# Kernel tuning notes

Measured on AMD Instinct MI355X. Metric: run time of the kernel, lower is better.

Reference implementation:

```python
import math
import jax, jax.numpy as jnp
import numpy as np

B, T, D, H = 2, 2048, 768, 12
DH = D // H
EPS = 1e-5


def setup_inputs() -> dict:
    key = jax.random.key(0)
    ks = jax.random.split(key, 8)
    s = 0.02
    x = jax.random.normal(ks[0], (B, T, D), dtype=jnp.float32)
    lengths = jax.random.randint(ks[1], (B,), T // 2, T + 1)
    lengths = lengths.at[0].set(T)  # ensure max(lengths)==T (static shape)
    return {
        'x': x,
        'lengths': lengths,
        'w_qkv': jax.random.normal(ks[2], (D, 3 * D), dtype=jnp.float32) * s,
        'b_qkv': jnp.zeros((3 * D,), jnp.float32),
        'w_proj': jax.random.normal(ks[3], (D, D), dtype=jnp.float32) * s,
        'b_proj': jnp.zeros((D,), jnp.float32),
        'ln1_g': jnp.ones((D,), jnp.float32),
        'ln1_b': jnp.zeros((D,), jnp.float32),
        'w_fc': jax.random.normal(ks[4], (D, 4 * D), dtype=jnp.float32) * s,
        'b_fc': jnp.zeros((4 * D,), jnp.float32),
        'w_out': jax.random.normal(ks[5], (4 * D, D), dtype=jnp.float32) * s,
        'b_out': jnp.zeros((D,), jnp.float32),
        'ln2_g': jnp.ones((D,), jnp.float32),
        'ln2_b': jnp.zeros((D,), jnp.float32),
    }


def _gelu(x):
    c = math.sqrt(2.0 / math.pi)
    return 0.5 * x * (1.0 + jnp.tanh(c * (x + 0.044715 * x * x * x)))


def _layernorm(x, g, b):
    mu = jnp.mean(x, axis=-1, keepdims=True)
    var = jnp.mean(jnp.square(x - mu), axis=-1, keepdims=True)
    return (x - mu) * jax.lax.rsqrt(var + EPS) * g + b


def _block(x, lengths, w_qkv, b_qkv, w_proj, b_proj, ln1_g, ln1_b,
           w_fc, b_fc, w_out, b_out, ln2_g, ln2_b):
    dt = x.dtype
    # [B, T] validity mask from ragged lengths
    pos = jnp.arange(T)
    mask = (pos[None, :] < lengths[:, None]).astype(dt)

    # --- SeqMultiHeadAttention (scale=False) ---
    qkv = x @ w_qkv + b_qkv  # [B, T, 3D]
    q, k, v = jnp.split(qkv, 3, axis=-1)

    def split_heads(t):  # [B,T,D] -> [B,H,T,DH]
        return t.reshape(B, T, H, DH).transpose(0, 2, 1, 3)

    q, k, v = split_heads(q), split_heads(k), split_heads(v)
    w = jnp.einsum('bhqd,bhkd->bhqk', q, k)  # [B,H,T,T]
    amask = (mask[:, None, :, None] * mask[:, None, None, :])  # [B,1,T,T]
    w = w * amask + (-1e9) * (1.0 - amask)
    w = jax.nn.softmax(w, axis=-1) * amask
    a = jnp.einsum('bhqk,bhkd->bhqd', w, v)  # [B,H,T,DH]
    a = a.transpose(0, 2, 1, 3).reshape(B, T, D)
    a = a @ w_proj + b_proj

    # --- SeqLayerNorm 1: pack/unpack == per-position LN, padding zeroed ---
    n = _layernorm(x + a, ln1_g, ln1_b) * mask[..., None]

    # --- MLP (gelu) ---
    m = _gelu(n @ w_fc + b_fc) @ w_out + b_out

    # --- SeqLayerNorm 2 ---
    h = _layernorm(n + m, ln2_g, ln2_b) * mask[..., None]
    return h


def reference(x, lengths, w_qkv, b_qkv, w_proj, b_proj, ln1_g, ln1_b,
              w_fc, b_fc, w_out, b_out, ln2_g, ln2_b):
    return _block(x, lengths, w_qkv, b_qkv, w_proj, b_proj, ln1_g, ln1_b,
                  w_fc, b_fc, w_out, b_out, ln2_g, ln2_b)
```

## Files before the change

kernel.cpp:

```cpp
#include <hip/hip_runtime.h>
#include <hip/hip_bf16.h>
#include <math.h>

constexpr int Bc  = 2;
constexpr int Tc  = 2048;
constexpr int Dc  = 768;
constexpr int Hc  = 12;
constexpr int DHc = 64;
constexpr int M_ROWS = Bc * Tc;
constexpr int D3  = 3 * Dc;
constexpr int D4  = 4 * Dc;

typedef __attribute__((ext_vector_type(8))) short short8;
typedef __attribute__((ext_vector_type(4))) float f32x4;

__device__ __forceinline__ unsigned short f2bf(float v) {
    union { __hip_bfloat16 b; unsigned short u; } cv;
    cv.b = __float2bfloat16(v);
    return cv.u;
}
__device__ __forceinline__ float bf2f(unsigned short u) {
    union { __hip_bfloat16 b; unsigned short u; } cv;
    cv.u = u;
    return __bfloat162float(cv.b);
}
__device__ __forceinline__ void bsplit(float v, unsigned short& h, unsigned short& l) {
    h = f2bf(v);
    l = f2bf(v - bf2f(h));
}

__device__ __forceinline__ float gelu_f(float x) {
    const float c = 0.79788456080286535588f;
    return 0.5f * x * (1.0f + tanhf(c * (x + 0.044715f * x * x * x)));
}

__device__ __forceinline__ void glds16(const unsigned short* g, unsigned short* l) {
    __builtin_amdgcn_global_load_lds(
        (const __attribute__((address_space(1))) void*)g,
        (__attribute__((address_space(3))) void*)l, 16, 0, 0);
}

__device__ __forceinline__ void tcast8(
    const float* __restrict__ w, int ldw,
    unsigned short* __restrict__ th, int K, int N, int idx)
{
    const int n  = idx % N;
    const int k0 = (idx / N) * 8;
    unsigned short hv[8];
#pragma unroll
    for (int j = 0; j < 8; ++j)
        hv[j] = f2bf(w[(size_t)(k0 + j) * ldw + n]);
    const size_t o = (size_t)n * K + k0;
    *(ushort4*)(th + o)     = make_ushort4(hv[0], hv[1], hv[2], hv[3]);
    *(ushort4*)(th + o + 4) = make_ushort4(hv[4], hv[5], hv[6], hv[7]);
}

__global__ __launch_bounds__(256) void prepare_kernel(
    const float* __restrict__ x,
    const float* __restrict__ w_qkv, const float* __restrict__ w_proj,
    const float* __restrict__ w_fc,  const float* __restrict__ w_out,
    unsigned short* __restrict__ xh,
    unsigned short* __restrict__ wqkvT, unsigned short* __restrict__ wprojT,
    unsigned short* __restrict__ wfcT,  unsigned short* __restrict__ woutT)
{
    int id = blockIdx.x * 256 + threadIdx.x;
    if (id < 786432) {
        const float4 v = *(const float4*)(x + (size_t)id * 4);
        *(ushort4*)(xh + (size_t)id * 4) =
            make_ushort4(f2bf(v.x), f2bf(v.y), f2bf(v.z), f2bf(v.w));
        return;
    }
    id -= 786432;
    if (id < 221184) { tcast8(w_qkv, D3, wqkvT, Dc, D3, id); return; }
    id -= 221184;
    if (id < 73728)  { tcast8(w_proj, Dc, wprojT, Dc, Dc, id); return; }
    id -= 73728;
    if (id < 294912) { tcast8(w_fc, D4, wfcT, Dc, D4, id); return; }
    id -= 294912;
    tcast8(w_out, Dc, woutT, D4, Dc, id);
}

template <int TM, int MODE>
__global__ __launch_bounds__(256) void gemm_bf16(
    const unsigned short* __restrict__ A,
    const unsigned short* __restrict__ B,
    const float* __restrict__ bias,
    float* __restrict__ C, unsigned short* __restrict__ Cb,
    int M, int N, int K)
{
    constexpr int MT  = TM / 32;
    constexpr int ISS = TM / 32 + 4;
    __shared__ unsigned short Ash[2][TM * 64];
    __shared__ unsigned short Bsh[2][128 * 64];

    const int tid  = threadIdx.x;
    const int n0   = blockIdx.x * 128;
    const int m0   = blockIdx.y * TM;
    const int wave = tid >> 6;
    const int lane = tid & 63;
    const int wm   = (wave >> 1) * (TM / 2);
    const int wn   = (wave & 1) * 64;
    const int lrow = lane & 15;
    const int quad = lane >> 4;
    const int swz  = lrow & 7;

    f32x4 acc[MT][4];
    const f32x4 zero = {0.f, 0.f, 0.f, 0.f};
#pragma unroll
    for (int i = 0; i < MT; ++i)
#pragma unroll
        for (int j = 0; j < 4; ++j) acc[i][j] = zero;

    const int l8r  = lane >> 3;
    const int csel = ((lane & 7) ^ l8r) * 8;

    const int nsteps = K >> 6;

    auto stage = [&](int t, int b) {
        const int ks = t << 6;
#pragma unroll
        for (int j = 0; j < TM / 32; ++j) {
            const int rbase = wave * (TM / 4) + j * 8;
            glds16(A + (size_t)(m0 + rbase + l8r) * K + ks + csel,
                   &Ash[b][rbase * 64]);
        }
#pragma unroll
        for (int j = 0; j < 4; ++j) {
            const int rbase = wave * 32 + j * 8;
            glds16(B + (size_t)(n0 + rbase + l8r) * K + ks + csel,
                   &Bsh[b][rbase * 64]);
        }
    };

    stage(0, 0);
    stage(1, 1);

    for (int s = 0; s < nsteps; ++s) {
        const int cur = s & 1;

        if (s + 1 < nsteps) {
            asm volatile("s_waitcnt vmcnt(%0)" :: "i"(ISS) : "memory");
        } else {
            asm volatile("s_waitcnt vmcnt(0)" ::: "memory");
        }
        __builtin_amdgcn_s_barrier();

#pragma unroll
        for (int kk = 0; kk < 2; ++kk) {
            short8 fa[MT], fb[4];
            const int cl = kk * 4 + quad;
            const int pc = (cl ^ swz) * 8;
#pragma unroll
            for (int t = 0; t < MT; ++t)
                fa[t] = *(const short8*)&Ash[cur][(wm + t * 16 + lrow) * 64 + pc];
#pragma unroll
            for (int t = 0; t < 4; ++t)
                fb[t] = *(const short8*)&Bsh[cur][(wn + t * 16 + lrow) * 64 + pc];
#pragma unroll
            for (int mt = 0; mt < MT; ++mt)
#pragma unroll
                for (int nt = 0; nt < 4; ++nt)
                    acc[mt][nt] = __builtin_amdgcn_mfma_f32_16x16x32_bf16(
                        fa[mt], fb[nt], acc[mt][nt], 0, 0, 0);
        }

        __builtin_amdgcn_s_barrier();
        if (s + 2 < nsteps) stage(s + 2, cur);
    }

#pragma unroll
    for (int mt = 0; mt < MT; ++mt) {
        const int rowb = m0 + wm + mt * 16 + quad * 4;
#pragma unroll
        for (int nt = 0; nt < 4; ++nt) {
            const int col = n0 + wn + nt * 16 + lrow;
            const float bv = bias[col];
#pragma unroll
            for (int r = 0; r < 4; ++r) {
                const size_t ci = (size_t)(rowb + r) * N + col;
                if (MODE == 0) {
                    C[ci] = acc[mt][nt][r] + bv;
                } else if (MODE == 1) {
                    Cb[ci] = f2bf(gelu_f(acc[mt][nt][r] + bv));
                } else {
                    Cb[ci] = f2bf(acc[mt][nt][r] + bv);
                }
            }
        }
    }
}

constexpr int KS  = 72;
constexpr int PS2 = 72;

__global__ __launch_bounds__(256) void flash_attn_bf16(
    const unsigned short* __restrict__ qkv,
    const int* __restrict__ lengths,
    unsigned short* __restrict__ oh)
{
    __shared__ unsigned short Kh[64 * KS];
    __shared__ unsigned short Vt[64 * KS];
    __shared__ unsigned short PfU[64 * PS2];

    const int tid  = threadIdx.x;
    const int wave = tid >> 6;
    const int lane = tid & 63;
    const int m    = lane & 15;
    const int quad = lane >> 4;

    const int nqt = Tc / 64;
    const int qt  = blockIdx.x % nqt;
    const int bh  = blockIdx.x / nqt;
    const int hh  = bh % Hc;
    const int b   = bh / Hc;
    const int len = lengths[b];
    const int q0  = qt * 64;
    const size_t rs = (size_t)D3;
    const unsigned short* base = qkv + (size_t)b * Tc * rs;
    const int qcol = hh * DHc;
    const int kcol = Dc + hh * DHc;
    const int vcol = 2 * Dc + hh * DHc;

    if (q0 >= len) {
#pragma unroll
        for (int r = 0; r < 4; ++r) {
            const int qrow = q0 + wave * 16 + quad * 4 + r;
            const size_t ob = (size_t)(b * Tc + qrow) * Dc + hh * DHc + m;
#pragma unroll
            for (int nt = 0; nt < 4; ++nt) oh[ob + nt * 16] = 0;
        }
        return;
    }

    const int ktEnd = (min(len, Tc) + 63) >> 6;

    short8 Qf[2];
#pragma unroll
    for (int ch = 0; ch < 2; ++ch) {
        const size_t ga = (size_t)(q0 + wave * 16 + m) * rs + qcol + ch * 32 + quad * 8;
        const short8 q8 = *(const short8*)&base[ga];
        short8 qs;
#pragma unroll
        for (int j = 0; j < 8; ++j)
            qs[j] = (short)f2bf(bf2f((unsigned short)q8[j]) * 1.44269504088896f);
        Qf[ch] = qs;
    }

    f32x4 Oacc[4];
    const f32x4 zero = {0.f, 0.f, 0.f, 0.f};
#pragma unroll
    for (int nt = 0; nt < 4; ++nt) Oacc[nt] = zero;
    float lrow[4] = {0.f, 0.f, 0.f, 0.f};

    const int kr0 = tid >> 3,          kc0 = (tid & 7) * 8;
    const int kr1 = (tid + 256) >> 3,  kc1 = ((tid + 256) & 7) * 8;
    const int pk  = (tid >> 4) * 4;
    const int pd  = (tid & 15) * 4;
    const int vswz = ((pk >> 3) ^ ((pd >> 2) & 7)) * 8 + (pk & 7);

    short8  pK0, pK1;
    ushort4 pV0, pV1, pV2, pV3;
    {
        pK0 = *(const short8*)&base[(size_t)kr0 * rs + kcol + kc0];
        pK1 = *(const short8*)&base[(size_t)kr1 * rs + kcol + kc1];
        pV0 = *(const ushort4*)&base[(size_t)(pk + 0) * rs + vcol + pd];
        pV1 = *(const ushort4*)&base[(size_t)(pk + 1) * rs + vcol + pd];
        pV2 = *(const ushort4*)&base[(size_t)(pk + 2) * rs + vcol + pd];
        pV3 = *(const ushort4*)&base[(size_t)(pk + 3) * rs + vcol + pd];
    }

    for (int kt = 0; kt < ktEnd; ++kt) {
        const int kbase = kt * 64;
        __syncthreads();

        *(short8*)&Kh[kr0 * KS + kc0] = pK0;
        *(short8*)&Kh[kr1 * KS + kc1] = pK1;
        *(ushort4*)&Vt[(pd + 0) * KS + vswz] = make_ushort4(pV0.x, pV1.x, pV2.x, pV3.x);
        *(ushort4*)&Vt[(pd + 1) * KS + vswz] = make_ushort4(pV0.y, pV1.y, pV2.y, pV3.y);
        *(ushort4*)&Vt[(pd + 2) * KS + vswz] = make_ushort4(pV0.z, pV1.z, pV2.z, pV3.z);
        *(ushort4*)&Vt[(pd + 3) * KS + vswz] = make_ushort4(pV0.w, pV1.w, pV2.w, pV3.w);
        __syncthreads();

        if (kt + 1 < ktEnd) {
            const int nb = kbase + 64;
            pK0 = *(const short8*)&base[(size_t)(nb + kr0) * rs + kcol + kc0];
            pK1 = *(const short8*)&base[(size_t)(nb + kr1) * rs + kcol + kc1];
            pV0 = *(const ushort4*)&base[(size_t)(nb + pk + 0) * rs + vcol + pd];
            pV1 = *(const ushort4*)&base[(size_t)(nb + pk + 1) * rs + vcol + pd];
            pV2 = *(const ushort4*)&base[(size_t)(nb + pk + 2) * rs + vcol + pd];
            pV3 = *(const ushort4*)&base[(size_t)(nb + pk + 3) * rs + vcol + pd];
        }

        f32x4 S4[4];
#pragma unroll
        for (int nt = 0; nt < 4; ++nt) S4[nt] = zero;
#pragma unroll
        for (int ch = 0; ch < 2; ++ch)
#pragma unroll
            for (int nt = 0; nt < 4; ++nt) {
                const short8 k8 = *(const short8*)&Kh[(nt * 16 + m) * KS + ch * 32 + quad * 8];
                S4[nt] = __builtin_amdgcn_mfma_f32_16x16x32_bf16(Qf[ch], k8, S4[nt], 0, 0, 0);
            }

        if (kbase + 64 > len) {
#pragma unroll
            for (int nt = 0; nt < 4; ++nt)
                if (kbase + nt * 16 + m >= len) {
#pragma unroll
                    for (int r = 0; r < 4; ++r) S4[nt][r] = -1e30f;
                }
        }

#pragma unroll
        for (int nt = 0; nt < 4; ++nt)
#pragma unroll
            for (int r = 0; r < 4; ++r) {
                const float p = __builtin_amdgcn_exp2f(S4[nt][r]);
                lrow[r] += p;
                PfU[(wave * 16 + quad * 4 + r) * PS2 + nt * 16 + m] = f2bf(p);
            }

#pragma unroll
        for (int ch = 0; ch < 2; ++ch) {
            const short8 P8 = *(const short8*)&PfU[(wave * 16 + m) * PS2 + ch * 32 + quad * 8];
#pragma unroll
            for (int nt = 0; nt < 4; ++nt) {
                const int pchunk = ((ch * 4 + quad) ^ ((nt * 4 + (m >> 2)) & 7)) * 8;
                const short8 v8 = *(const short8*)&Vt[(nt * 16 + m) * KS + pchunk];
                Oacc[nt] = __builtin_amdgcn_mfma_f32_16x16x32_bf16(P8, v8, Oacc[nt], 0, 0, 0);
            }
        }
    }

#pragma unroll
    for (int r = 0; r < 4; ++r) {
#pragma unroll
        for (int sh = 8; sh >= 1; sh >>= 1)
            lrow[r] += __shfl_xor(lrow[r], sh);
    }

#pragma unroll
    for (int r = 0; r < 4; ++r) {
        const int qrow = q0 + wave * 16 + quad * 4 + r;
        const size_t ob = (size_t)(b * Tc + qrow) * Dc + hh * DHc + m;
        if (qrow < len) {
            const float inv = 1.0f / lrow[r];
#pragma unroll
            for (int nt = 0; nt < 4; ++nt)
                oh[ob + nt * 16] = f2bf(Oacc[nt][r] * inv);
        } else {
#pragma unroll
            for (int nt = 0; nt < 4; ++nt)
                oh[ob + nt * 16] = 0;
        }
    }
}

__global__ __launch_bounds__(256) void ln_split_kernel(
    const float* __restrict__ X, const float* __restrict__ Y,
    const float* __restrict__ g, const float* __restrict__ beta,
    const int* __restrict__ lengths,
    unsigned short* __restrict__ outh, unsigned short* __restrict__ outl)
{
    __shared__ float red[4];
    const int row = blockIdx.x;
    const int b = row / Tc, t = row % Tc;
    const int len = lengths[b];
    const size_t basei = (size_t)row * Dc;
    const int tid = threadIdx.x;

    if (t >= len) {
        for (int j = tid; j < Dc; j += 256) { outh[basei + j] = 0; outl[basei + j] = 0; }
        return;
    }

    float v[3];
    float s = 0.f;
#pragma unroll
    for (int j = 0; j < 3; ++j) {
        int idx = tid + j * 256;
        v[j] = X[basei + idx] + Y[basei + idx];
        s += v[j];
    }
    const int lane = tid % 64, wid = tid / 64;
#pragma unroll
    for (int sh = 32; sh >= 1; sh >>= 1) s += __shfl_xor(s, sh);
    if (lane == 0) red[wid] = s;
    __syncthreads();
    s = red[0] + red[1] + red[2] + red[3];
    const float mu = s * (1.0f / Dc);

    float vs = 0.f;
#pragma unroll
    for (int j = 0; j < 3; ++j) { float dv = v[j] - mu; vs += dv * dv; }
    __syncthreads();
#pragma unroll
    for (int sh = 32; sh >= 1; sh >>= 1) vs += __shfl_xor(vs, sh);
    if (lane == 0) red[wid] = vs;
    __syncthreads();
    vs = red[0] + red[1] + red[2] + red[3];
    const float rstd = rsqrtf(vs * (1.0f / Dc) + 1e-5f);

#pragma unroll
    for (int j = 0; j < 3; ++j) {
        int idx = tid + j * 256;
        const float ov = (v[j] - mu) * rstd * g[idx] + beta[idx];
        unsigned short hh, ll;
        bsplit(ov, hh, ll);
        outh[basei + idx] = hh;
        outl[basei + idx] = ll;
    }
}

__global__ __launch_bounds__(256) void ln2_kernel(
    const unsigned short* __restrict__ Xh, const unsigned short* __restrict__ Xl,
    const float* Y,
    const float* __restrict__ g, const float* __restrict__ beta,
    const int* __restrict__ lengths, float* out)
{
    __shared__ float red[4];
    const int row = blockIdx.x;
    const int b = row / Tc, t = row % Tc;
    const int len = lengths[b];
    const size_t basei = (size_t)row * Dc;
    const int tid = threadIdx.x;

    if (t >= len) {
        for (int j = tid; j < Dc; j += 256) out[basei + j] = 0.f;
        return;
    }

    float v[3];
    float s = 0.f;
#pragma unroll
    for (int j = 0; j < 3; ++j) {
        int idx = tid + j * 256;
        v[j] = bf2f(Xh[basei + idx]) + bf2f(Xl[basei + idx]) + Y[basei + idx];
        s += v[j];
    }
    const int lane = tid % 64, wid = tid / 64;
#pragma unroll
    for (int sh = 32; sh >= 1; sh >>= 1) s += __shfl_xor(s, sh);
    if (lane == 0) red[wid] = s;
    __syncthreads();
    s = red[0] + red[1] + red[2] + red[3];
    const float mu = s * (1.0f / Dc);

    float vs = 0.f;
#pragma unroll
    for (int j = 0; j < 3; ++j) { float dv = v[j] - mu; vs += dv * dv; }
    __syncthreads();
#pragma unroll
    for (int sh = 32; sh >= 1; sh >>= 1) vs += __shfl_xor(vs, sh);
    if (lane == 0) red[wid] = vs;
    __syncthreads();
    vs = red[0] + red[1] + red[2] + red[3];
    const float rstd = rsqrtf(vs * (1.0f / Dc) + 1e-5f);

#pragma unroll
    for (int j = 0; j < 3; ++j) {
        int idx = tid + j * 256;
        out[basei + idx] = (v[j] - mu) * rstd * g[idx] + beta[idx];
    }
}

extern "C" void kernel_launch(void* const* d_in, const int* in_sizes, int n_in,
                              void* d_out, int out_size, void* d_ws, size_t ws_size,
                              hipStream_t stream)
{
    const float* x      = (const float*)d_in[0];
    const int*   lens   = (const int*)  d_in[1];
    const float* w_qkv  = (const float*)d_in[2];
    const float* b_qkv  = (const float*)d_in[3];
    const float* w_proj = (const float*)d_in[4];
    const float* b_proj = (const float*)d_in[5];
    const float* ln1_g  = (const float*)d_in[6];
    const float* ln1_b  = (const float*)d_in[7];
    const float* w_fc   = (const float*)d_in[8];
    const float* b_fc   = (const float*)d_in[9];
    const float* w_out  = (const float*)d_in[10];
    const float* b_out  = (const float*)d_in[11];
    const float* ln2_g  = (const float*)d_in[12];
    const float* ln2_b  = (const float*)d_in[13];

    if (ws_size < 51904512) return;

    char* ws = (char*)d_ws;
    unsigned short* qkvh  = (unsigned short*)(ws + 0);
    unsigned short* xh    = (unsigned short*)(ws + 18874368);
    unsigned short* ah    = xh;
    float*          projo = (float*)(ws + 0);
    unsigned short* fH    = (unsigned short*)(ws + 0);
    unsigned short* nh    = (unsigned short*)(ws + 25165824);
    unsigned short* nl    = (unsigned short*)(ws + 31457280);
    unsigned short* wqkvT = (unsigned short*)(ws + 37748736);
    unsigned short* wprojT= (unsigned short*)(ws + 41287680);
    unsigned short* wfcT  = (unsigned short*)(ws + 42467328);
    unsigned short* woutT = (unsigned short*)(ws + 47185920);
    float*          mbuf  = (float*)d_out;

    const dim3 blk(256);

    prepare_kernel<<<dim3(6528), blk, 0, stream>>>(
        x, w_qkv, w_proj, w_fc, w_out, xh, wqkvT, wprojT, wfcT, woutT);

    gemm_bf16<128, 3><<<dim3(D3 / 128, M_ROWS / 128), blk, 0, stream>>>(
        xh, wqkvT, b_qkv, nullptr, qkvh, M_ROWS, D3, Dc);

    flash_attn_bf16<<<dim3(Bc * Hc * (Tc / 64)), blk, 0, stream>>>(qkvh, lens, ah);

    gemm_bf16<64, 0><<<dim3(Dc / 128, M_ROWS / 64), blk, 0, stream>>>(
        ah, wprojT, b_proj, projo, nullptr, M_ROWS, Dc, Dc);

    ln_split_kernel<<<dim3(M_ROWS), blk, 0, stream>>>(x, projo, ln1_g, ln1_b, lens, nh, nl);

    gemm_bf16<128, 1><<<dim3(D4 / 128, M_ROWS / 128), blk, 0, stream>>>(
        nh, wfcT, b_fc, nullptr, fH, M_ROWS, D4, Dc);

    gemm_bf16<64, 0><<<dim3(Dc / 128, M_ROWS / 64), blk, 0, stream>>>(
        fH, woutT, b_out, mbuf, nullptr, M_ROWS, Dc, D4);

    ln2_kernel<<<dim3(M_ROWS), blk, 0, stream>>>(nh, nl, mbuf, ln2_g, ln2_b, lens,
                                                 (float*)d_out);
}
```

Before: 317.9 us.

## Use 256x256 8-wave GEMM tiles with XCD remap and double-buffer attention K/V

```diff
diff --git a/kernel.cpp b/kernel.cpp
--- a/kernel.cpp
+++ b/kernel.cpp
@@ -80,34 +80,37 @@
     tcast8(w_out, Dc, woutT, D4, Dc, id);
 }
 
-template <int TM, int MODE>
-__global__ __launch_bounds__(256) void gemm_bf16(
+template <int MODE>
+__global__ __launch_bounds__(512) void gemm256p8(
     const unsigned short* __restrict__ A,
     const unsigned short* __restrict__ B,
     const float* __restrict__ bias,
     float* __restrict__ C, unsigned short* __restrict__ Cb,
-    int M, int N, int K)
-{
-    constexpr int MT  = TM / 32;
-    constexpr int ISS = TM / 32 + 4;
-    __shared__ unsigned short Ash[2][TM * 64];
-    __shared__ unsigned short Bsh[2][128 * 64];
+    int N, int K)
+{
+    __shared__ unsigned short Ash[2][256 * 64];
+    __shared__ unsigned short Bsh[2][256 * 64];
 
     const int tid  = threadIdx.x;
-    const int n0   = blockIdx.x * 128;
-    const int m0   = blockIdx.y * TM;
     const int wave = tid >> 6;
     const int lane = tid & 63;
-    const int wm   = (wave >> 1) * (TM / 2);
-    const int wn   = (wave & 1) * 64;
+
+    const int nper = gridDim.x >> 3;
+    const int gid  = (blockIdx.x & 7) * nper + (blockIdx.x >> 3);
+    const int bx   = gid / 16;
+    const int by   = gid % 16;
+    const int m0 = by * 256, n0 = bx * 256;
+
+    const int wm   = (wave >> 2) * 128;
+    const int wn   = (wave & 3) * 64;
     const int lrow = lane & 15;
     const int quad = lane >> 4;
     const int swz  = lrow & 7;
 
-    f32x4 acc[MT][4];
+    f32x4 acc[8][4];
     const f32x4 zero = {0.f, 0.f, 0.f, 0.f};
 #pragma unroll
-    for (int i = 0; i < MT; ++i)
+    for (int i = 0; i < 8; ++i)
 #pragma unroll
         for (int j = 0; j < 4; ++j) acc[i][j] = zero;
 
@@ -116,60 +119,75 @@
 
     const int nsteps = K >> 6;
 
-    auto stage = [&](int t, int b) {
-        const int ks = t << 6;
-#pragma unroll
-        for (int j = 0; j < TM / 32; ++j) {
-            const int rbase = wave * (TM / 4) + j * 8;
-            glds16(A + (size_t)(m0 + rbase + l8r) * K + ks + csel,
-                   &Ash[b][rbase * 64]);
-        }
-#pragma unroll
-        for (int j = 0; j < 4; ++j) {
-            const int rbase = wave * 32 + j * 8;
-            glds16(B + (size_t)(n0 + rbase + l8r) * K + ks + csel,
-                   &Bsh[b][rbase * 64]);
-        }
-    };
-
-    stage(0, 0);
-    stage(1, 1);
+#pragma unroll
+    for (int j = 0; j < 4; ++j) {
+        const int rb = wave * 32 + j * 8;
+        glds16(A + (size_t)(m0 + rb + l8r) * K + csel, &Ash[0][rb * 64]);
+        glds16(B + (size_t)(n0 + rb + l8r) * K + csel, &Bsh[0][rb * 64]);
+    }
+    asm volatile("s_waitcnt vmcnt(0)" ::: "memory");
+    __builtin_amdgcn_s_barrier();
+    __builtin_amdgcn_sched_barrier(0);
 
     for (int s = 0; s < nsteps; ++s) {
         const int cur = s & 1;
-
-        if (s + 1 < nsteps) {
-            asm volatile("s_waitcnt vmcnt(%0)" :: "i"(ISS) : "memory");
-        } else {
-            asm volatile("s_waitcnt vmcnt(0)" ::: "memory");
-        }
+        const int nxt = cur ^ 1;
+        const bool pf = (s + 1 < nsteps);
+        const int ksn = (s + 1) << 6;
+
+#pragma unroll
+        for (int p = 0; p < 4; ++p) {
+            const int mh = (p >> 1) * 4;
+            const int nh = (p & 1) * 2;
+
+            short8 fa[4][2], fb[2][2];
+#pragma unroll
+            for (int kk = 0; kk < 2; ++kk) {
+                const int pc = ((kk * 4 + quad) ^ swz) * 8;
+#pragma unroll
+                for (int i = 0; i < 4; ++i)
+                    fa[i][kk] = *(const short8*)
+                        &Ash[cur][(wm + (mh + i) * 16 + lrow) * 64 + pc];
+#pragma unroll
+                for (int j = 0; j < 2; ++j)
+                    fb[j][kk] = *(const short8*)
+                        &Bsh[cur][(wn + (nh + j) * 16 + lrow) * 64 + pc];
+            }
+
+            if (pf && p < 2) {
+#pragma unroll
+                for (int j = 0; j < 2; ++j) {
+                    const int rb = wave * 32 + (p * 2 + j) * 8;
+                    glds16(A + (size_t)(m0 + rb + l8r) * K + ksn + csel,
+                           &Ash[nxt][rb * 64]);
+                    glds16(B + (size_t)(n0 + rb + l8r) * K + ksn + csel,
+                           &Bsh[nxt][rb * 64]);
+                }
+            }
+
+            __builtin_amdgcn_s_barrier();
+
+            __builtin_amdgcn_s_setprio(1);
+#pragma unroll
+            for (int kk = 0; kk < 2; ++kk)
+#pragma unroll
+                for (int i = 0; i < 4; ++i)
+#pragma unroll
+                    for (int j = 0; j < 2; ++j)
+                        acc[mh + i][nh + j] = __builtin_amdgcn_mfma_f32_16x16x32_bf16(
+                            fa[i][kk], fb[j][kk], acc[mh + i][nh + j], 0, 0, 0);
+            __builtin_amdgcn_s_setprio(0);
+
+            if (p < 3) __builtin_amdgcn_s_barrier();
+        }
+
+        asm volatile("s_waitcnt vmcnt(0)" ::: "memory");
         __builtin_amdgcn_s_barrier();
-
-#pragma unroll
-        for (int kk = 0; kk < 2; ++kk) {
-            short8 fa[MT], fb[4];
-            const int cl = kk * 4 + quad;
-            const int pc = (cl ^ swz) * 8;
-#pragma unroll
-            for (int t = 0; t < MT; ++t)
-                fa[t] = *(const short8*)&Ash[cur][(wm + t * 16 + lrow) * 64 + pc];
-#pragma unroll
-            for (int t = 0; t < 4; ++t)
-                fb[t] = *(const short8*)&Bsh[cur][(wn + t * 16 + lrow) * 64 + pc];
-#pragma unroll
-            for (int mt = 0; mt < MT; ++mt)
-#pragma unroll
-                for (int nt = 0; nt < 4; ++nt)
-                    acc[mt][nt] = __builtin_amdgcn_mfma_f32_16x16x32_bf16(
-                        fa[mt], fb[nt], acc[mt][nt], 0, 0, 0);
-        }
-
-        __builtin_amdgcn_s_barrier();
-        if (s + 2 < nsteps) stage(s + 2, cur);
-    }
-
-#pragma unroll
-    for (int mt = 0; mt < MT; ++mt) {
+        __builtin_amdgcn_sched_barrier(0);
+    }
+
+#pragma unroll
+    for (int mt = 0; mt < 8; ++mt) {
         const int rowb = m0 + wm + mt * 16 + quad * 4;
 #pragma unroll
         for (int nt = 0; nt < 4; ++nt) {
@@ -198,8 +216,8 @@
     const int* __restrict__ lengths,
     unsigned short* __restrict__ oh)
 {
-    __shared__ unsigned short Kh[64 * KS];
-    __shared__ unsigned short Vt[64 * KS];
+    __shared__ unsigned short Kh[2][64 * KS];
+    __shared__ unsigned short Vt[2][64 * KS];
     __shared__ unsigned short PfU[64 * PS2];
 
     const int tid  = threadIdx.x;
@@ -271,14 +289,14 @@
 
     for (int kt = 0; kt < ktEnd; ++kt) {
         const int kbase = kt * 64;
-        __syncthreads();
-
-        *(short8*)&Kh[kr0 * KS + kc0] = pK0;
-        *(short8*)&Kh[kr1 * KS + kc1] = pK1;
-        *(ushort4*)&Vt[(pd + 0) * KS + vswz] = make_ushort4(pV0.x, pV1.x, pV2.x, pV3.x);
-        *(ushort4*)&Vt[(pd + 1) * KS + vswz] = make_ushort4(pV0.y, pV1.y, pV2.y, pV3.y);
-        *(ushort4*)&Vt[(pd + 2) * KS + vswz] = make_ushort4(pV0.z, pV1.z, pV2.z, pV3.z);
-        *(ushort4*)&Vt[(pd + 3) * KS + vswz] = make_ushort4(pV0.w, pV1.w, pV2.w, pV3.w);
+        const int c = kt & 1;
+
+        *(short8*)&Kh[c][kr0 * KS + kc0] = pK0;
+        *(short8*)&Kh[c][kr1 * KS + kc1] = pK1;
+        *(ushort4*)&Vt[c][(pd + 0) * KS + vswz] = make_ushort4(pV0.x, pV1.x, pV2.x, pV3.x);
+        *(ushort4*)&Vt[c][(pd + 1) * KS + vswz] = make_ushort4(pV0.y, pV1.y, pV2.y, pV3.y);
+        *(ushort4*)&Vt[c][(pd + 2) * KS + vswz] = make_ushort4(pV0.z, pV1.z, pV2.z, pV3.z);
+        *(ushort4*)&Vt[c][(pd + 3) * KS + vswz] = make_ushort4(pV0.w, pV1.w, pV2.w, pV3.w);
         __syncthreads();
 
         if (kt + 1 < ktEnd) {
@@ -294,13 +312,15 @@
         f32x4 S4[4];
 #pragma unroll
         for (int nt = 0; nt < 4; ++nt) S4[nt] = zero;
+        __builtin_amdgcn_s_setprio(1);
 #pragma unroll
         for (int ch = 0; ch < 2; ++ch)
 #pragma unroll
             for (int nt = 0; nt < 4; ++nt) {
-                const short8 k8 = *(const short8*)&Kh[(nt * 16 + m) * KS + ch * 32 + quad * 8];
+                const short8 k8 = *(const short8*)&Kh[c][(nt * 16 + m) * KS + ch * 32 + quad * 8];
                 S4[nt] = __builtin_amdgcn_mfma_f32_16x16x32_bf16(Qf[ch], k8, S4[nt], 0, 0, 0);
             }
+        __builtin_amdgcn_s_setprio(0);
 
         if (kbase + 64 > len) {
 #pragma unroll
@@ -323,12 +343,14 @@
 #pragma unroll
         for (int ch = 0; ch < 2; ++ch) {
             const short8 P8 = *(const short8*)&PfU[(wave * 16 + m) * PS2 + ch * 32 + quad * 8];
+            __builtin_amdgcn_s_setprio(1);
 #pragma unroll
             for (int nt = 0; nt < 4; ++nt) {
                 const int pchunk = ((ch * 4 + quad) ^ ((nt * 4 + (m >> 2)) & 7)) * 8;
-                const short8 v8 = *(const short8*)&Vt[(nt * 16 + m) * KS + pchunk];
+                const short8 v8 = *(const short8*)&Vt[c][(nt * 16 + m) * KS + pchunk];
                 Oacc[nt] = __builtin_amdgcn_mfma_f32_16x16x32_bf16(P8, v8, Oacc[nt], 0, 0, 0);
             }
+            __builtin_amdgcn_s_setprio(0);
         }
     }
 
@@ -500,25 +522,26 @@
     float*          mbuf  = (float*)d_out;
 
     const dim3 blk(256);
+    const dim3 blk512(512);
 
     prepare_kernel<<<dim3(6528), blk, 0, stream>>>(
         x, w_qkv, w_proj, w_fc, w_out, xh, wqkvT, wprojT, wfcT, woutT);
 
-    gemm_bf16<128, 3><<<dim3(D3 / 128, M_ROWS / 128), blk, 0, stream>>>(
-        xh, wqkvT, b_qkv, nullptr, qkvh, M_ROWS, D3, Dc);
+    gemm256p8<3><<<dim3((D3 / 256) * 16), blk512, 0, stream>>>(
+        xh, wqkvT, b_qkv, nullptr, qkvh, D3, Dc);
 
     flash_attn_bf16<<<dim3(Bc * Hc * (Tc / 64)), blk, 0, stream>>>(qkvh, lens, ah);
 
-    gemm_bf16<64, 0><<<dim3(Dc / 128, M_ROWS / 64), blk, 0, stream>>>(
-        ah, wprojT, b_proj, projo, nullptr, M_ROWS, Dc, Dc);
+    gemm256p8<0><<<dim3((Dc / 256) * 16), blk512, 0, stream>>>(
+        ah, wprojT, b_proj, projo, nullptr, Dc, Dc);
 
     ln_split_kernel<<<dim3(M_ROWS), blk, 0, stream>>>(x, projo, ln1_g, ln1_b, lens, nh, nl);
 
-    gemm_bf16<128, 1><<<dim3(D4 / 128, M_ROWS / 128), blk, 0, stream>>>(
-        nh, wfcT, b_fc, nullptr, fH, M_ROWS, D4, Dc);
-
-    gemm_bf16<64, 0><<<dim3(Dc / 128, M_ROWS / 64), blk, 0, stream>>>(
-        fH, woutT, b_out, mbuf, nullptr, M_ROWS, Dc, D4);
+    gemm256p8<1><<<dim3((D4 / 256) * 16), blk512, 0, stream>>>(
+        nh, wfcT, b_fc, nullptr, fH, D4, Dc);
+
+    gemm256p8<0><<<dim3((Dc / 256) * 16), blk512, 0, stream>>>(
+        fH, woutT, b_out, mbuf, nullptr, Dc, D4);
 
     ln2_kernel<<<dim3(M_ROWS), blk, 0, stream>>>(nh, nl, mbuf, ln2_g, ln2_b, lens,
                                                  (float*)d_out);
```

New measurement: 386.6 us. 1.22x slower.
